# Kernel optimization log

Hardware: AMD Instinct MI355X
Metric: run time of the kernel (lower is better)

The kernel has to match this reference:

```python
import jax, jax.numpy as jnp
import numpy as np

B, C_IN, S = 32, 4, 2048
NF = 256          # CNN filters
H = 256           # LSTM hidden per direction
NH, DH = 8, 64    # heads, single-head size
MH = 512          # multihead size
KSZ, PAD, POOL = 13, 6, 6
SP = (S + 2 * PAD - KSZ + 1) // POOL  # 341: post conv(len-preserving)+maxpool1d length


def _lstm_dir(x, Wih, Whh, b):
    # x: [T, N, C] -- torch LSTM gate order i,f,g,o; b = b_ih + b_hh merged
    N = x.shape[1]
    h0 = jnp.zeros((N, H), x.dtype)
    c0 = jnp.zeros((N, H), x.dtype)

    def step(carry, xt):
        h, c = carry
        g = xt @ Wih.T + h @ Whh.T + b
        i, f, gg, o = jnp.split(g, 4, axis=-1)
        c = jax.nn.sigmoid(f) * c + jax.nn.sigmoid(i) * jnp.tanh(gg)
        h = jax.nn.sigmoid(o) * jnp.tanh(c)
        return (h, c), h

    _, hs = jax.lax.scan(step, (h0, c0), x)
    return hs


def _bilstm(x, Wih, Whh, b):
    fwd = _lstm_dir(x, Wih[0], Whh[0], b[0])
    bwd = _lstm_dir(x[::-1], Wih[1], Whh[1], b[1])[::-1]
    return jnp.concatenate([fwd, bwd], axis=-1)


def _rpe():
    # RelativePosition: |clip(k-q, -(S-1), S-1)| / (S-1); identical across the
    # batch-repeat channels, so compute once then broadcast (same math).
    r = jnp.arange(S)
    d = jnp.abs(jnp.clip(r[None, :] - r[:, None], -(S - 1), S - 1))
    d = d.astype(jnp.float32) / jnp.float32(S - 1)
    # nn.MaxPool2d((9,9), stride=(6,6), padding=1) -> [341, 341]
    return jax.lax.reduce_window(d, -jnp.inf, jax.lax.max, (9, 9), (6, 6), [(1, 1), (1, 1)])


def setup_inputs():
    key = jax.random.key(0)
    ks = jax.random.split(key, 20)
    f = lambda i, shape: jax.random.normal(ks[i], shape, jnp.float32) * 0.05
    return {
        "inputs": jax.random.normal(ks[0], (B, C_IN, S), jnp.float32),
        "conv1_w": f(1, (NF, C_IN, KSZ)),
        "bn1_gamma": jnp.ones((NF,), jnp.float32),
        "bn1_beta": jnp.zeros((NF,), jnp.float32),
        "Wih0": f(2, (2, 4 * H, NF)),
        "Whh0": f(3, (2, 4 * H, H)),
        "b0": f(4, (2, 4 * H)),
        "Wih1": f(5, (2, 4 * H, 2 * H)),
        "Whh1": f(6, (2, 4 * H, H)),
        "b1": f(7, (2, 4 * H)),
        "Qw": f(8, (NH, DH, 2 * H)), "Qb": f(9, (NH, DH)),
        "Kw": f(10, (NH, DH, 2 * H)), "Kb": f(11, (NH, DH)),
        "Vw": f(12, (NH, DH, 2 * H)), "Vb": f(13, (NH, DH)),
        "mh_w": f(14, (MH, NH * DH)), "mh_b": f(15, (MH,)),
    }


def reference(inputs, conv1_w, bn1_gamma, bn1_beta, Wih0, Whh0, b0,
              Wih1, Whh1, b1, Qw, Qb, Kw, Kb, Vw, Vb, mh_w, mh_b):
    # layer1: Conv1d (bias=False, pad=6 keeps length) + BatchNorm1d(eval: mean=0, var=1) + ReLU + MaxPool1d(6)
    x = jax.lax.conv_general_dilated(inputs, conv1_w, (1,), [(PAD, PAD)],
                                     dimension_numbers=('NCH', 'OIH', 'NCH'))
    x = x * (bn1_gamma / jnp.sqrt(1.0 + 1e-5))[None, :, None] + bn1_beta[None, :, None]
    x = jax.nn.relu(x)
    x = jax.lax.reduce_window(x, -jnp.inf, jax.lax.max, (1, 1, POOL), (1, 1, POOL), 'VALID')  # [B,NF,SP]
    x = jnp.transpose(x, (0, 2, 1))  # [B, SP, NF]

    # torch nn.LSTM with batch_first=False fed [B,SP,NF]: scans over axis 0 (batch) -- replicated faithfully.
    x = _bilstm(x, Wih0, Whh0, b0)
    x = _bilstm(x, Wih1, Whh1, b1)  # [B, SP, 2H]
    # (the F_RNN/R_RNN split-and-concat is an identity)

    # per-head Q/K/V (batched over heads), relative attention, dropout off (eval)
    q = jnp.einsum('bsc,hdc->hbsd', x, Qw) + Qb[:, None, None, :]
    k = jnp.einsum('bsc,hdc->hbsd', x, Kw) + Kb[:, None, None, :]
    v = jnp.einsum('bsc,hdc->hbsd', x, Vw) + Vb[:, None, None, :]
    scores = jnp.einsum('hbqd,hbkd->hbqk', q, k) / jnp.sqrt(jnp.float32(DH))
    scores = scores / _rpe()[None, None, :, :]
    p = jax.nn.softmax(scores, axis=-1)
    attn = jax.nn.relu(jnp.einsum('hbqk,hbkd->hbqd', p, v))  # [NH,B,SP,DH]
    cat = jnp.transpose(attn, (1, 2, 0, 3)).reshape(B, SP, NH * DH)
    out = jax.nn.relu(cat @ mh_w.T + mh_b)  # MultiHeadLinear + MHReLU
    return out
```

## Files before the change

kernel.cpp:

```cpp
#include <hip/hip_runtime.h>
#include <math.h>

#define B_    32
#define CIN   4
#define SLEN  2048
#define NF    256
#define HD    256
#define SP    341
#define RTOT  (B_*SP)
#define NH_   8
#define DH_   64
#define GRP   4
#define PSTR  344
#define HS    (SP*HD)
#define NBLK  176

typedef __attribute__((ext_vector_type(8))) short short8;
typedef __attribute__((ext_vector_type(4))) float floatx4;
typedef __attribute__((ext_vector_type(4))) unsigned short ushortx4;
typedef __attribute__((ext_vector_type(8))) unsigned short ushort8;

__device__ __forceinline__ float sigmoidf_(float x) { return 1.0f / (1.0f + expf(-x)); }

__device__ __forceinline__ unsigned short f2bf(float x) {
    unsigned int u = __float_as_uint(x);
    unsigned int r = (u + 0x7FFF + ((u >> 16) & 1)) >> 16;
    return (unsigned short)r;
}
__device__ __forceinline__ float bf2f(unsigned short b) {
    return __uint_as_float(((unsigned int)b) << 16);
}

__device__ __forceinline__ void store_f4_llc(float* p, floatx4 v)
{
    asm volatile("global_store_dwordx4 %0, %1, off sc0 sc1" :: "v"(p), "v"(v) : "memory");
}
__device__ __forceinline__ unsigned load_u32_llc(const unsigned* p)
{
    unsigned r;
    asm volatile("global_load_dword %0, %1, off sc0 sc1\n\ts_waitcnt vmcnt(0)"
                 : "=v"(r) : "v"(p) : "memory");
    return r;
}
__device__ __forceinline__ void load_h16_llc(const float* p, floatx4* r)
{
    asm volatile(
        "global_load_dwordx4 %0, %16, off sc0 sc1\n\t"
        "global_load_dwordx4 %1, %16, off offset:16 sc0 sc1\n\t"
        "global_load_dwordx4 %2, %16, off offset:128 sc0 sc1\n\t"
        "global_load_dwordx4 %3, %16, off offset:144 sc0 sc1\n\t"
        "global_load_dwordx4 %4, %16, off offset:256 sc0 sc1\n\t"
        "global_load_dwordx4 %5, %16, off offset:272 sc0 sc1\n\t"
        "global_load_dwordx4 %6, %16, off offset:384 sc0 sc1\n\t"
        "global_load_dwordx4 %7, %16, off offset:400 sc0 sc1\n\t"
        "global_load_dwordx4 %8, %16, off offset:512 sc0 sc1\n\t"
        "global_load_dwordx4 %9, %16, off offset:528 sc0 sc1\n\t"
        "global_load_dwordx4 %10, %16, off offset:640 sc0 sc1\n\t"
        "global_load_dwordx4 %11, %16, off offset:656 sc0 sc1\n\t"
        "global_load_dwordx4 %12, %16, off offset:768 sc0 sc1\n\t"
        "global_load_dwordx4 %13, %16, off offset:784 sc0 sc1\n\t"
        "global_load_dwordx4 %14, %16, off offset:896 sc0 sc1\n\t"
        "global_load_dwordx4 %15, %16, off offset:912 sc0 sc1\n\t"
        "s_waitcnt vmcnt(0)"
        : "=&v"(r[0]), "=&v"(r[1]), "=&v"(r[2]), "=&v"(r[3]),
          "=&v"(r[4]), "=&v"(r[5]), "=&v"(r[6]), "=&v"(r[7]),
          "=&v"(r[8]), "=&v"(r[9]), "=&v"(r[10]), "=&v"(r[11]),
          "=&v"(r[12]), "=&v"(r[13]), "=&v"(r[14]), "=&v"(r[15])
        : "v"(p)
        : "memory");
}


__global__ __launch_bounds__(256)
void conv_pool_k(const float* __restrict__ in, const float* __restrict__ cw,
                 const float* __restrict__ gamma, const float* __restrict__ beta,
                 unsigned short* __restrict__ x0p)
{
    const int b  = blockIdx.y;
    const int s0 = blockIdx.x * 16;
    const int co = threadIdx.x;
    __shared__ float ins[CIN][16*6 + 12];
    for (int idx = threadIdx.x; idx < CIN*108; idx += 256) {
        int ci = idx / 108, o = idx % 108;
        int pos = 6*s0 - 6 + o;
        ins[ci][o] = (pos >= 0 && pos < SLEN) ? in[(b*CIN + ci)*SLEN + pos] : 0.0f;
    }
    float wreg[52];
    {
        const float4* wp = (const float4*)(cw + co*52);
        #pragma unroll
        for (int j4 = 0; j4 < 13; ++j4) {
            float4 w4 = wp[j4];
            wreg[j4*4+0]=w4.x; wreg[j4*4+1]=w4.y; wreg[j4*4+2]=w4.z; wreg[j4*4+3]=w4.w;
        }
    }
    const float scale = gamma[co] * (1.0f / sqrtf(1.0f + 1e-5f));
    const float shift = beta[co];
    __syncthreads();
    for (int si = 0; si < 16; ++si) {
        int s = s0 + si;
        if (s >= SP) break;
        float win[CIN][18];
        #pragma unroll
        for (int ci = 0; ci < CIN; ++ci)
            #pragma unroll
            for (int o = 0; o < 18; ++o)
                win[ci][o] = ins[ci][6*si + o];
        float m = -1e30f;
        #pragma unroll
        for (int p6 = 0; p6 < 6; ++p6) {
            float acc = 0.0f;
            #pragma unroll
            for (int ci = 0; ci < CIN; ++ci)
                #pragma unroll
                for (int kk = 0; kk < 13; ++kk)
                    acc += win[ci][p6+kk] * wreg[ci*13+kk];
            float val = acc * scale + shift;
            val = fmaxf(val, 0.0f);
            m = fmaxf(m, val);
        }
        unsigned short hb_ = f2bf(m);
        unsigned short lb_ = f2bf(m - bf2f(hb_));
        size_t rb = (size_t)(b*SP + s)*512 + (size_t)(co >> 3)*16 + (co & 7);
        x0p[rb]     = hb_;
        x0p[rb + 8] = lb_;
    }
}

__global__ __launch_bounds__(256)
void pack4_k(const float* __restrict__ W, unsigned short* __restrict__ hi,
             unsigned short* __restrict__ lo, int n4)
{
    int i = blockIdx.x * 256 + threadIdx.x;
    if (i >= n4) return;
    float4 x = *((const float4*)W + i);
    float v[4] = {x.x, x.y, x.z, x.w};
    ushortx4 h, l;
    #pragma unroll
    for (int e = 0; e < 4; ++e) {
        unsigned short hb = f2bf(v[e]);
        h[e] = hb;
        l[e] = f2bf(v[e] - bf2f(hb));
    }
    *((ushortx4*)hi + i) = h;
    *((ushortx4*)lo + i) = l;
}

__global__ __launch_bounds__(256)
void pack8_k(const float* __restrict__ W, unsigned short* __restrict__ O, int n8)
{
    int i = blockIdx.x * 256 + threadIdx.x;
    if (i >= n8) return;
    const float4* wp = (const float4*)W + (size_t)i*2;
    float4 a = wp[0], b = wp[1];
    float v[8] = {a.x,a.y,a.z,a.w,b.x,b.y,b.z,b.w};
    ushort8 h, l;
    #pragma unroll
    for (int e = 0; e < 8; ++e) {
        unsigned short hb = f2bf(v[e]);
        h[e] = hb;
        l[e] = f2bf(v[e] - bf2f(hb));
    }
    *(ushort8*)(O + (size_t)i*16)     = h;
    *(ushort8*)(O + (size_t)i*16 + 8) = l;
}

template<int RELU>
__global__ __launch_bounds__(256)
void gemm_bf_k(const unsigned short* __restrict__ Ap, const unsigned short* __restrict__ Bp,
               const float* __restrict__ bias, float* __restrict__ C,
               int M, int N, int K)
{
    const int n0 = blockIdx.x * 128;
    const int m0 = blockIdx.y * 128;
    const int tid = threadIdx.x;
    const int lane = tid & 63;
    const int w = tid >> 6;
    const int wm = w >> 1, wn = w & 1;
    const int ln15 = lane & 15, lq = lane >> 4;
    const int l8 = lane >> 3, lj = lane & 7;
    const size_t rstr = 2*(size_t)K;

    __shared__ unsigned short As[128*64];
    __shared__ unsigned short Bs[128*64];

    floatx4 acc[4][4];
    #pragma unroll
    for (int i = 0; i < 4; ++i)
        #pragma unroll
        for (int j = 0; j < 4; ++j) acc[i][j] = (floatx4){0.f, 0.f, 0.f, 0.f};

    int rloc[4];
    #pragma unroll
    for (int c = 0; c < 4; ++c) rloc[c] = w*32 + c*8 + l8;
    const int spos = lj ^ (l8 & 7);

    for (int k0 = 0; k0 < K; k0 += 32) {
        short8 va[4], vb[4];
        #pragma unroll
        for (int c = 0; c < 4; ++c) {
            int gra = m0 + rloc[c]; if (gra >= M) gra = M - 1;
            va[c] = *(const short8*)(Ap + (size_t)gra*rstr + k0*2 + lj*8);
            vb[c] = *(const short8*)(Bp + (size_t)(n0 + rloc[c])*rstr + k0*2 + lj*8);
        }
        __syncthreads();
        #pragma unroll
        for (int c = 0; c < 4; ++c) {
            *(short8*)&As[rloc[c]*64 + spos*8] = va[c];
            *(short8*)&Bs[rloc[c]*64 + spos*8] = vb[c];
        }
        __syncthreads();

        short8 fa_h[4], fa_l[4], fb_h[4], fb_l[4];
        #pragma unroll
        for (int mt = 0; mt < 4; ++mt) {
            const int lr = wm*64 + mt*16 + ln15;
            fa_h[mt] = *(const short8*)&As[lr*64 + (((lq*2  ) ^ (lr&7))*8)];
            fa_l[mt] = *(const short8*)&As[lr*64 + (((lq*2+1) ^ (lr&7))*8)];
        }
        #pragma unroll
        for (int nt = 0; nt < 4; ++nt) {
            const int lr = wn*64 + nt*16 + ln15;
            fb_h[nt] = *(const short8*)&Bs[lr*64 + (((lq*2  ) ^ (lr&7))*8)];
            fb_l[nt] = *(const short8*)&Bs[lr*64 + (((lq*2+1) ^ (lr&7))*8)];
        }
        #pragma unroll
        for (int mt = 0; mt < 4; ++mt)
            #pragma unroll
            for (int nt = 0; nt < 4; ++nt) {
                acc[mt][nt] = __builtin_amdgcn_mfma_f32_16x16x32_bf16(fa_l[mt], fb_h[nt], acc[mt][nt], 0, 0, 0);
                acc[mt][nt] = __builtin_amdgcn_mfma_f32_16x16x32_bf16(fa_h[mt], fb_l[nt], acc[mt][nt], 0, 0, 0);
                acc[mt][nt] = __builtin_amdgcn_mfma_f32_16x16x32_bf16(fa_h[mt], fb_h[nt], acc[mt][nt], 0, 0, 0);
            }
    }

    #pragma unroll
    for (int nt = 0; nt < 4; ++nt) {
        const int n = n0 + wn*64 + nt*16 + ln15;
        const float bv = bias[n];
        #pragma unroll
        for (int mt = 0; mt < 4; ++mt) {
            const int mbase = m0 + wm*64 + mt*16 + lq*4;
            #pragma unroll
            for (int r = 0; r < 4; ++r) {
                int m = mbase + r;
                if (m < M) {
                    float val = acc[mt][nt][r] + bv;
                    if (RELU) val = fmaxf(val, 0.0f);
                    C[(size_t)m*N + n] = val;
                }
            }
        }
    }
}

__global__ __launch_bounds__(256)
void lstm_scan_k(const float* __restrict__ G,
                 const unsigned short* __restrict__ Whi,
                 const unsigned short* __restrict__ Wlo,
                 float* __restrict__ hb,
                 unsigned short* __restrict__ x_out,
                 unsigned* __restrict__ bar)
{
    const int j0 = blockIdx.x * 32;
    const int m0 = blockIdx.y * 32;
    const int d  = blockIdx.z;
    const int tid = threadIdx.x;
    const int w = tid >> 6, lane = tid & 63;
    const int mhalf = w & 1, gpair = w >> 1;
    const int ln15 = lane & 15, lq = lane >> 4;
    const size_t hsz = (size_t)2*SP*HD;
    unsigned* gbar = bar + (size_t)(blockIdx.y*2 + blockIdx.z)*64;

    __shared__ float Csh[32][132];

    int am = m0 + mhalf*16 + ln15; if (am > SP-1) am = SP-1;
    const int akoff = lq * 8;

    const unsigned short* WhiD = Whi + (size_t)d*1024*256;
    const unsigned short* WloD = Wlo + (size_t)d*1024*256;
    int nrow[4];
    #pragma unroll
    for (int t = 0; t < 4; ++t)
        nrow[t] = (gpair*2 + (t>>1))*256 + j0 + (t&1)*16 + ln15;

    const int emloc = tid >> 3;
    const int ej4   = (tid & 7) * 4;
    const int em    = m0 + emloc;

    floatx4 creg = (floatx4){0.f, 0.f, 0.f, 0.f};

    for (int s = 0; s < B_; ++s) {
        const int t_in = d ? (B_ - 1 - s) : s;
        float* hbuf_in  = hb + (size_t)(s & 1)*hsz;
        float* hbuf_out = hb + (size_t)((s+1) & 1)*hsz;

        floatx4 acc[4];
        #pragma unroll
        for (int t = 0; t < 4; ++t) acc[t] = (floatx4){0.f, 0.f, 0.f, 0.f};

        if (s > 0) {
            const float* p = hbuf_in + (size_t)d*HS + (size_t)am*HD + akoff;
            floatx4 hr[16];
            load_h16_llc(p, hr);
            #pragma unroll
            for (int kk = 0; kk < 8; ++kk) {
                const int ko = kk*32 + akoff;
                float vv[8] = {hr[2*kk][0], hr[2*kk][1], hr[2*kk][2], hr[2*kk][3],
                               hr[2*kk+1][0], hr[2*kk+1][1], hr[2*kk+1][2], hr[2*kk+1][3]};
                short8 ahi, alo;
                #pragma unroll
                for (int e = 0; e < 8; ++e) {
                    unsigned short hb16 = f2bf(vv[e]);
                    ahi[e] = (short)hb16;
                    alo[e] = (short)f2bf(vv[e] - bf2f(hb16));
                }
                #pragma unroll
                for (int t = 0; t < 4; ++t) {
                    short8 bhi = *(const short8*)(WhiD + (size_t)nrow[t]*HD + ko);
                    short8 blo = *(const short8*)(WloD + (size_t)nrow[t]*HD + ko);
                    acc[t] = __builtin_amdgcn_mfma_f32_16x16x32_bf16(alo, bhi, acc[t], 0, 0, 0);
                    acc[t] = __builtin_amdgcn_mfma_f32_16x16x32_bf16(ahi, blo, acc[t], 0, 0, 0);
                    acc[t] = __builtin_amdgcn_mfma_f32_16x16x32_bf16(ahi, bhi, acc[t], 0, 0, 0);
                }
            }
        }

        #pragma unroll
        for (int t = 0; t < 4; ++t) {
            int col = gpair*64 + (t>>1)*32 + (t&1)*16 + ln15;
            int rb  = mhalf*16 + lq*4;
            #pragma unroll
            for (int r = 0; r < 4; ++r)
                Csh[rb + r][col] = acc[t][r];
        }
        __syncthreads();

        if (em < SP) {
            size_t gb = ((size_t)t_in*SP + em)*2048 + (size_t)d*1024 + j0 + ej4;
            float4 gi4 = *(const float4*)&G[gb];
            float4 gf4 = *(const float4*)&G[gb + 256];
            float4 gg4 = *(const float4*)&G[gb + 512];
            float4 go4 = *(const float4*)&G[gb + 768];
            float hv[4];
            #pragma unroll
            for (int e = 0; e < 4; ++e) {
                float gi = Csh[emloc][     ej4+e] + (&gi4.x)[e];
                float gf = Csh[emloc][32 + ej4+e] + (&gf4.x)[e];
                float gg = Csh[emloc][64 + ej4+e] + (&gg4.x)[e];
                float go = Csh[emloc][96 + ej4+e] + (&go4.x)[e];
                float cn = sigmoidf_(gf)*creg[e] + sigmoidf_(gi)*tanhf(gg);
                creg[e] = cn;
                hv[e] = sigmoidf_(go)*tanhf(cn);
            }
            size_t cbase = ((size_t)d*SP + em)*HD + j0 + ej4;
            floatx4 ho = (floatx4){hv[0], hv[1], hv[2], hv[3]};
            store_f4_llc(&hbuf_out[cbase], ho);
            const int colg = d*HD + j0 + ej4;
            size_t xb = ((size_t)t_in*SP + em)*1024 + (size_t)(colg >> 3)*16 + (colg & 7);
            ushortx4 xh, xl;
            #pragma unroll
            for (int e = 0; e < 4; ++e) {
                unsigned short hb16 = f2bf(hv[e]);
                xh[e] = hb16;
                xl[e] = f2bf(hv[e] - bf2f(hb16));
            }
            *(ushortx4*)&x_out[xb]     = xh;
            *(ushortx4*)&x_out[xb + 8] = xl;
        }

        if (s < B_ - 1) {
            asm volatile("s_waitcnt vmcnt(0)" ::: "memory");
            __syncthreads();
            if (tid == 0) {
                atomicAdd(gbar, 1u);
                const unsigned target = (unsigned)(s + 1) * 8u;
                while (load_u32_llc(gbar) < target)
                    __builtin_amdgcn_s_sleep(2);
            }
            __syncthreads();
        }
    }
}

__global__ __launch_bounds__(256)
void scores_k(const float* __restrict__ q, const float* __restrict__ k,
              float* __restrict__ P, int g)
{
    const int h = blockIdx.z, bl = blockIdx.y, bg = g*GRP + bl;
    const int q0 = (blockIdx.x / 6) * 64;
    const int k0 = (blockIdx.x % 6) * 64;
    const int tid = threadIdx.x;
    __shared__ float qs[64][68];
    __shared__ float ks[64][68];
    {
        int jr = tid >> 2, c16 = (tid & 3) * 16;
        int qq = q0 + jr; if (qq > SP-1) qq = SP-1;
        int kr = k0 + jr; if (kr > SP-1) kr = SP-1;
        const float* qp = &q[((size_t)bg*SP + qq)*512 + h*64 + c16];
        const float* kp = &k[((size_t)bg*SP + kr)*512 + h*64 + c16];
        #pragma unroll
        for (int u = 0; u < 4; ++u) {
            *(float4*)&qs[jr][c16 + u*4] = *(const float4*)(qp + u*4);
            *(float4*)&ks[jr][c16 + u*4] = *(const float4*)(kp + u*4);
        }
    }
    __syncthreads();
    const int tx = tid & 15, ty = tid >> 4;
    float acc[4][4];
    #pragma unroll
    for (int i = 0; i < 4; ++i)
        #pragma unroll
        for (int j = 0; j < 4; ++j) acc[i][j] = 0.0f;
    for (int d4 = 0; d4 < 64; d4 += 4) {
        float4 a[4], b[4];
        #pragma unroll
        for (int i = 0; i < 4; ++i) a[i] = *(const float4*)&qs[ty + 16*i][d4];
        #pragma unroll
        for (int j = 0; j < 4; ++j) b[j] = *(const float4*)&ks[tx + 16*j][d4];
        #pragma unroll
        for (int i = 0; i < 4; ++i)
            #pragma unroll
            for (int j = 0; j < 4; ++j)
                acc[i][j] += a[i].x*b[j].x + a[i].y*b[j].y + a[i].z*b[j].z + a[i].w*b[j].w;
    }
    #pragma unroll
    for (int i = 0; i < 4; ++i) {
        int qq = q0 + ty + 16*i;
        if (qq >= SP) continue;
        int r0 = 6*qq - 1; if (r0 < 0) r0 = 0;
        int r1 = 6*qq + 7; if (r1 > SLEN-1) r1 = SLEN-1;
        size_t rowb = ((size_t)(h*GRP + bl)*SP + qq) * PSTR;
        #pragma unroll
        for (int j = 0; j < 4; ++j) {
            int kk = k0 + tx + 16*j;
            if (kk >= SP) continue;
            int c0 = 6*kk - 1; if (c0 < 0) c0 = 0;
            int c1 = 6*kk + 7;
            int dd1 = c1 - r0; if (dd1 < 0) dd1 = -dd1;
            int dd2 = r1 - c0; if (dd2 < 0) dd2 = -dd2;
            int den = dd1 > dd2 ? dd1 : dd2;
            P[rowb + kk] = (acc[i][j] * 0.125f) * 2047.0f / (float)den;
        }
    }
}

__global__ __launch_bounds__(256)
void softmax_k(float* __restrict__ P)
{
    const int tid = threadIdx.x;
    const int row = blockIdx.x * 4 + (tid >> 6);
    const int lane = tid & 63;
    float* rp = P + (size_t)row * PSTR;
    float v[6];
    float m = -1e30f;
    #pragma unroll
    for (int i = 0; i < 6; ++i) {
        int col = lane + 64*i;
        v[i] = (col < SP) ? rp[col] : -1e30f;
        m = fmaxf(m, v[i]);
    }
    #pragma unroll
    for (int o = 1; o < 64; o <<= 1) m = fmaxf(m, __shfl_xor(m, o, 64));
    float s = 0.0f;
    #pragma unroll
    for (int i = 0; i < 6; ++i) {
        v[i] = expf(v[i] - m);
        s += v[i];
    }
    #pragma unroll
    for (int o = 1; o < 64; o <<= 1) s += __shfl_xor(s, o, 64);
    float inv = 1.0f / s;
    #pragma unroll
    for (int i = 0; i < 6; ++i) {
        int col = lane + 64*i;
        if (col < SP) rp[col] = v[i] * inv;
    }
}

__global__ __launch_bounds__(256)
void pv_k(const float* __restrict__ P, const float* __restrict__ v,
          unsigned short* __restrict__ catp, int g)
{
    const int h = blockIdx.z, bl = blockIdx.y, bg = g*GRP + bl;
    const int q0 = blockIdx.x * 64;
    const int tid = threadIdx.x;
    __shared__ float ps[64][68];
    __shared__ float vs[64][68];
    const int tx = tid & 15, ty = tid >> 4;
    float acc[4][4];
    #pragma unroll
    for (int i = 0; i < 4; ++i)
        #pragma unroll
        for (int j = 0; j < 4; ++j) acc[i][j] = 0.0f;

    for (int kc = 0; kc < 6; ++kc) {
        const int kk0 = kc * 64;
        {
            int jr = tid >> 2, c16 = (tid & 3) * 16;
            int qq = q0 + jr; if (qq > SP-1) qq = SP-1;
            const float* pp = P + ((size_t)(h*GRP + bl)*SP + qq)*PSTR + kk0 + c16;
            #pragma unroll
            for (int u = 0; u < 4; ++u) {
                float4 w = *(const float4*)(pp + u*4);
                int klb = c16 + u*4;
                float vals[4] = {w.x, w.y, w.z, w.w};
                #pragma unroll
                for (int e = 0; e < 4; ++e)
                    ps[klb + e][jr] = (kk0 + klb + e < SP) ? vals[e] : 0.0f;
            }
        }
        {
            int jr = tid >> 2, c16 = (tid & 3) * 16;
            int kr = kk0 + jr; if (kr > SP-1) kr = SP-1;
            const float* vp = &v[((size_t)bg*SP + kr)*512 + h*64 + c16];
            #pragma unroll
            for (int u = 0; u < 4; ++u)
                *(float4*)&vs[jr][c16 + u*4] = *(const float4*)(vp + u*4);
        }
        __syncthreads();
        for (int kk = 0; kk < 64; ++kk) {
            float4 a4 = *(const float4*)&ps[kk][ty*4];
            float4 b4 = *(const float4*)&vs[kk][tx*4];
            float av[4] = {a4.x, a4.y, a4.z, a4.w};
            float bv[4] = {b4.x, b4.y, b4.z, b4.w};
            #pragma unroll
            for (int i = 0; i < 4; ++i)
                #pragma unroll
                for (int j = 0; j < 4; ++j)
                    acc[i][j] += av[i] * bv[j];
        }
        __syncthreads();
    }
    #pragma unroll
    for (int i = 0; i < 4; ++i) {
        int qq = q0 + ty*4 + i;
        if (qq >= SP) continue;
        float r[4];
        r[0] = fmaxf(acc[i][0], 0.0f);
        r[1] = fmaxf(acc[i][1], 0.0f);
        r[2] = fmaxf(acc[i][2], 0.0f);
        r[3] = fmaxf(acc[i][3], 0.0f);
        const int colg = h*64 + tx*4;
        size_t xb = ((size_t)bg*SP + qq)*1024 + (size_t)(colg >> 3)*16 + (colg & 7);
        ushortx4 xh, xl;
        #pragma unroll
        for (int e = 0; e < 4; ++e) {
            unsigned short hb16 = f2bf(r[e]);
            xh[e] = hb16;
            xl[e] = f2bf(r[e] - bf2f(hb16));
        }
        *(ushortx4*)&catp[xb]     = xh;
        *(ushortx4*)&catp[xb + 8] = xl;
    }
}

extern "C" void kernel_launch(void* const* d_in, const int* in_sizes, int n_in,
                              void* d_out, int out_size, void* d_ws, size_t ws_size,
                              hipStream_t stream)
{
    (void)in_sizes; (void)n_in; (void)out_size; (void)ws_size;
    const float* in    = (const float*)d_in[0];
    const float* cw    = (const float*)d_in[1];
    const float* gamma = (const float*)d_in[2];
    const float* beta  = (const float*)d_in[3];
    const float* Wih0  = (const float*)d_in[4];
    const float* Whh0  = (const float*)d_in[5];
    const float* b0    = (const float*)d_in[6];
    const float* Wih1  = (const float*)d_in[7];
    const float* Whh1  = (const float*)d_in[8];
    const float* b1    = (const float*)d_in[9];
    const float* Qw    = (const float*)d_in[10];
    const float* Qb    = (const float*)d_in[11];
    const float* Kw    = (const float*)d_in[12];
    const float* Kb    = (const float*)d_in[13];
    const float* Vw    = (const float*)d_in[14];
    const float* Vb    = (const float*)d_in[15];
    const float* mhw   = (const float*)d_in[16];
    const float* mhb   = (const float*)d_in[17];
    float* out = (float*)d_out;

    float* x0 = (float*)d_ws;
    float* G  = x0 + (size_t)RTOT*NF;
    float* x1 = G  + (size_t)RTOT*2048;
    float* x2 = x1 + (size_t)RTOT*512;
    float* hb = x2 + (size_t)RTOT*512;
    float* cb = hb + (size_t)2*2*SP*HD;

    float* qbuf = G;
    float* kbuf = G + (size_t)RTOT*512;
    float* vbuf = G + (size_t)2*RTOT*512;
    float* P    = G + (size_t)3*RTOT*512;
    unsigned* bar = (unsigned*)cb;

    unsigned short* x0p = (unsigned short*)x0;
    unsigned short* whh1_hi = (unsigned short*)x0;
    unsigned short* whh1_lo = whh1_hi + (size_t)524288;
    unsigned short* wih0_p  = (unsigned short*)x2;
    unsigned short* wih1_p  = wih0_p + (size_t)1048576;
    unsigned short* whh0_hi = wih1_p + (size_t)2097152;
    unsigned short* whh0_lo = whh0_hi + (size_t)524288;
    unsigned short* x1p  = (unsigned short*)x1;
    unsigned short* catp = (unsigned short*)x1;
    unsigned short* x2p = (unsigned short*)x2;
    float* gslack = P + (size_t)NH_*GRP*SP*PSTR;
    unsigned short* qw_p = (unsigned short*)gslack;
    unsigned short* kw_p = qw_p + (size_t)524288;
    unsigned short* vw_p = kw_p + (size_t)524288;
    unsigned short* mw_p = vw_p + (size_t)524288;

    #define PACKGRID(n) dim3(((n) + 255) / 256)

    conv_pool_k<<<dim3(22, B_), 256, 0, stream>>>(in, cw, gamma, beta, x0p);
    pack8_k<<<PACKGRID(65536), 256, 0, stream>>>(Wih0, wih0_p, 65536);
    gemm_bf_k<0><<<dim3(16, 86), 256, 0, stream>>>(x0p, wih0_p, b0, G, RTOT, 2048, 256);
    pack4_k<<<PACKGRID(131072), 256, 0, stream>>>(Whh0, whh0_hi, whh0_lo, 131072);
    pack4_k<<<PACKGRID(131072), 256, 0, stream>>>(Whh1, whh1_hi, whh1_lo, 131072);
    pack8_k<<<PACKGRID(131072), 256, 0, stream>>>(Wih1, wih1_p, 131072);
    hipMemsetAsync(bar, 0, 22*64*sizeof(unsigned), stream);
    {
        const float* a0 = G; const unsigned short* a1 = whh0_hi; const unsigned short* a2 = whh0_lo;
        float* a3 = hb; unsigned short* a4 = x1p; unsigned* a5 = bar;
        void* kargs[] = {&a0, &a1, &a2, &a3, &a4, &a5};
        hipLaunchCooperativeKernel((void*)lstm_scan_k, dim3(8, 11, 2), dim3(256, 1, 1), kargs, 0, stream);
    }
    gemm_bf_k<0><<<dim3(16, 86), 256, 0, stream>>>(x1p, wih1_p, b1, G, RTOT, 2048, 512);
    hipMemsetAsync(bar, 0, 22*64*sizeof(unsigned), stream);
    {
        const float* a0 = G; const unsigned short* a1 = whh1_hi; const unsigned short* a2 = whh1_lo;
        float* a3 = hb; unsigned short* a4 = x2p; unsigned* a5 = bar;
        void* kargs[] = {&a0, &a1, &a2, &a3, &a4, &a5};
        hipLaunchCooperativeKernel((void*)lstm_scan_k, dim3(8, 11, 2), dim3(256, 1, 1), kargs, 0, stream);
    }
    pack8_k<<<PACKGRID(32768), 256, 0, stream>>>(Qw,  qw_p, 32768);
    pack8_k<<<PACKGRID(32768), 256, 0, stream>>>(Kw,  kw_p, 32768);
    pack8_k<<<PACKGRID(32768), 256, 0, stream>>>(Vw,  vw_p, 32768);
    pack8_k<<<PACKGRID(32768), 256, 0, stream>>>(mhw, mw_p, 32768);
    gemm_bf_k<0><<<dim3(4, 86), 256, 0, stream>>>(x2p, qw_p, Qb, qbuf, RTOT, 512, 512);
    gemm_bf_k<0><<<dim3(4, 86), 256, 0, stream>>>(x2p, kw_p, Kb, kbuf, RTOT, 512, 512);
    gemm_bf_k<0><<<dim3(4, 86), 256, 0, stream>>>(x2p, vw_p, Vb, vbuf, RTOT, 512, 512);
    for (int g = 0; g < B_/GRP; ++g) {
        scores_k <<<dim3(36, GRP, NH_), 256, 0, stream>>>(qbuf, kbuf, P, g);
        softmax_k<<<dim3(NH_*GRP*SP/4), 256, 0, stream>>>(P);
        pv_k     <<<dim3(6, GRP, NH_), 256, 0, stream>>>(P, vbuf, catp, g);
    }
    gemm_bf_k<1><<<dim3(4, 86), 256, 0, stream>>>(catp, mw_p, mhb, out, RTOT, 512, 512);
    #undef PACKGRID
}
```

Before: 1.643 ms.

## Fuse scores with softmax and move PV to split-bf16 MFMA with transposed V

Merges the score computation and the row softmax into one kernel that holds a full 341-column row in registers, so the separate softmax pass and its fp32 round trip are dropped. P is written in a packed hi/lo bf16 layout, and V is written transposed in the same packed form by a new GEMM epilogue. The PV product now runs on bf16 MFMA with three passes to recover near-fp32 precision. This adds a memset over the transposed V buffer. The scores kernel now launches fewer, larger blocks that loop over all key chunks, which may lower parallelism.

```diff
diff --git a/kernel.cpp b/kernel.cpp
--- a/kernel.cpp
+++ b/kernel.cpp
@@ -13,7 +13,7 @@
 #define GRP   4
 #define PSTR  344
 #define HS    (SP*HD)
-#define NBLK  176
+#define PKS   768
 
 typedef __attribute__((ext_vector_type(8))) short short8;
 typedef __attribute__((ext_vector_type(4))) float floatx4;
@@ -255,6 +255,98 @@
 }
 
 __global__ __launch_bounds__(256)
+void gemm_vT_k(const unsigned short* __restrict__ Ap, const unsigned short* __restrict__ Bp,
+               const float* __restrict__ bias, unsigned short* __restrict__ vT,
+               int M, int N, int K)
+{
+    const int n0 = blockIdx.x * 128;
+    const int m0 = blockIdx.y * 128;
+    const int tid = threadIdx.x;
+    const int lane = tid & 63;
+    const int w = tid >> 6;
+    const int wm = w >> 1, wn = w & 1;
+    const int ln15 = lane & 15, lq = lane >> 4;
+    const int l8 = lane >> 3, lj = lane & 7;
+    const size_t rstr = 2*(size_t)K;
+
+    __shared__ unsigned short As[128*64];
+    __shared__ unsigned short Bs[128*64];
+
+    floatx4 acc[4][4];
+    #pragma unroll
+    for (int i = 0; i < 4; ++i)
+        #pragma unroll
+        for (int j = 0; j < 4; ++j) acc[i][j] = (floatx4){0.f, 0.f, 0.f, 0.f};
+
+    int rloc[4];
+    #pragma unroll
+    for (int c = 0; c < 4; ++c) rloc[c] = w*32 + c*8 + l8;
+    const int spos = lj ^ (l8 & 7);
+
+    for (int k0 = 0; k0 < K; k0 += 32) {
+        short8 va[4], vb[4];
+        #pragma unroll
+        for (int c = 0; c < 4; ++c) {
+            int gra = m0 + rloc[c]; if (gra >= M) gra = M - 1;
+            va[c] = *(const short8*)(Ap + (size_t)gra*rstr + k0*2 + lj*8);
+            vb[c] = *(const short8*)(Bp + (size_t)(n0 + rloc[c])*rstr + k0*2 + lj*8);
+        }
+        __syncthreads();
+        #pragma unroll
+        for (int c = 0; c < 4; ++c) {
+            *(short8*)&As[rloc[c]*64 + spos*8] = va[c];
+            *(short8*)&Bs[rloc[c]*64 + spos*8] = vb[c];
+        }
+        __syncthreads();
+
+        short8 fa_h[4], fa_l[4], fb_h[4], fb_l[4];
+        #pragma unroll
+        for (int mt = 0; mt < 4; ++mt) {
+            const int lr = wm*64 + mt*16 + ln15;
+            fa_h[mt] = *(const short8*)&As[lr*64 + (((lq*2  ) ^ (lr&7))*8)];
+            fa_l[mt] = *(const short8*)&As[lr*64 + (((lq*2+1) ^ (lr&7))*8)];
+        }
+        #pragma unroll
+        for (int nt = 0; nt < 4; ++nt) {
+            const int lr = wn*64 + nt*16 + ln15;
+            fb_h[nt] = *(const short8*)&Bs[lr*64 + (((lq*2  ) ^ (lr&7))*8)];
+            fb_l[nt] = *(const short8*)&Bs[lr*64 + (((lq*2+1) ^ (lr&7))*8)];
+        }
+        #pragma unroll
+        for (int mt = 0; mt < 4; ++mt)
+            #pragma unroll
+            for (int nt = 0; nt < 4; ++nt) {
+                acc[mt][nt] = __builtin_amdgcn_mfma_f32_16x16x32_bf16(fa_l[mt], fb_h[nt], acc[mt][nt], 0, 0, 0);
+                acc[mt][nt] = __builtin_amdgcn_mfma_f32_16x16x32_bf16(fa_h[mt], fb_l[nt], acc[mt][nt], 0, 0, 0);
+                acc[mt][nt] = __builtin_amdgcn_mfma_f32_16x16x32_bf16(fa_h[mt], fb_h[nt], acc[mt][nt], 0, 0, 0);
+            }
+    }
+
+    #pragma unroll
+    for (int nt = 0; nt < 4; ++nt) {
+        const int n = n0 + wn*64 + nt*16 + ln15;
+        const float bv = bias[n];
+        #pragma unroll
+        for (int mt = 0; mt < 4; ++mt) {
+            const int mbase = m0 + wm*64 + mt*16 + lq*4;
+            #pragma unroll
+            for (int r = 0; r < 4; ++r) {
+                int m = mbase + r;
+                if (m < M) {
+                    float val = acc[mt][nt][r] + bv;
+                    int bg = m / 341;
+                    int sp = m - bg*341;
+                    size_t vb_ = ((size_t)bg*512 + n)*PKS + (size_t)((sp >> 3)*16 + (sp & 7));
+                    unsigned short hb16 = f2bf(val);
+                    vT[vb_]     = hb16;
+                    vT[vb_ + 8] = f2bf(val - bf2f(hb16));
+                }
+            }
+        }
+    }
+}
+
+__global__ __launch_bounds__(256)
 void lstm_scan_k(const float* __restrict__ G,
                  const unsigned short* __restrict__ Whi,
                  const unsigned short* __restrict__ Wlo,
@@ -384,174 +476,164 @@
 }
 
 __global__ __launch_bounds__(256)
-void scores_k(const float* __restrict__ q, const float* __restrict__ k,
-              float* __restrict__ P, int g)
+void scores_sm_k(const float* __restrict__ q, const float* __restrict__ k,
+                 unsigned short* __restrict__ Ppk, int g)
 {
     const int h = blockIdx.z, bl = blockIdx.y, bg = g*GRP + bl;
-    const int q0 = (blockIdx.x / 6) * 64;
-    const int k0 = (blockIdx.x % 6) * 64;
+    const int q0 = blockIdx.x * 32;
     const int tid = threadIdx.x;
-    __shared__ float qs[64][68];
+    const int tx = tid & 15, ty = tid >> 4;
+    __shared__ float qs[32][68];
     __shared__ float ks[64][68];
     {
-        int jr = tid >> 2, c16 = (tid & 3) * 16;
+        int jr = tid >> 3, c8 = (tid & 7) * 8;
         int qq = q0 + jr; if (qq > SP-1) qq = SP-1;
-        int kr = k0 + jr; if (kr > SP-1) kr = SP-1;
-        const float* qp = &q[((size_t)bg*SP + qq)*512 + h*64 + c16];
-        const float* kp = &k[((size_t)bg*SP + kr)*512 + h*64 + c16];
-        #pragma unroll
-        for (int u = 0; u < 4; ++u) {
-            *(float4*)&qs[jr][c16 + u*4] = *(const float4*)(qp + u*4);
-            *(float4*)&ks[jr][c16 + u*4] = *(const float4*)(kp + u*4);
-        }
-    }
-    __syncthreads();
-    const int tx = tid & 15, ty = tid >> 4;
-    float acc[4][4];
-    #pragma unroll
-    for (int i = 0; i < 4; ++i)
-        #pragma unroll
-        for (int j = 0; j < 4; ++j) acc[i][j] = 0.0f;
-    for (int d4 = 0; d4 < 64; d4 += 4) {
-        float4 a[4], b[4];
-        #pragma unroll
-        for (int i = 0; i < 4; ++i) a[i] = *(const float4*)&qs[ty + 16*i][d4];
-        #pragma unroll
-        for (int j = 0; j < 4; ++j) b[j] = *(const float4*)&ks[tx + 16*j][d4];
-        #pragma unroll
-        for (int i = 0; i < 4; ++i)
-            #pragma unroll
-            for (int j = 0; j < 4; ++j)
-                acc[i][j] += a[i].x*b[j].x + a[i].y*b[j].y + a[i].z*b[j].z + a[i].w*b[j].w;
-    }
-    #pragma unroll
-    for (int i = 0; i < 4; ++i) {
-        int qq = q0 + ty + 16*i;
-        if (qq >= SP) continue;
+        const float* qp = &q[((size_t)bg*SP + qq)*512 + h*64 + c8];
+        *(float4*)&qs[jr][c8]     = *(const float4*)qp;
+        *(float4*)&qs[jr][c8 + 4] = *(const float4*)(qp + 4);
+    }
+    float sv[2][24];
+    for (int kc = 0; kc < 6; ++kc) {
+        __syncthreads();
+        {
+            int jr = tid >> 2, c16 = (tid & 3) * 16;
+            int kr = kc*64 + jr; if (kr > SP-1) kr = SP-1;
+            const float* kp = &k[((size_t)bg*SP + kr)*512 + h*64 + c16];
+            #pragma unroll
+            for (int u = 0; u < 4; ++u)
+                *(float4*)&ks[jr][c16 + u*4] = *(const float4*)(kp + u*4);
+        }
+        __syncthreads();
+        float a_[2][4] = {{0.f,0.f,0.f,0.f},{0.f,0.f,0.f,0.f}};
+        for (int d4 = 0; d4 < 64; d4 += 4) {
+            float4 a0 = *(const float4*)&qs[ty][d4];
+            float4 a1 = *(const float4*)&qs[ty + 16][d4];
+            float4 b[4];
+            #pragma unroll
+            for (int j = 0; j < 4; ++j) b[j] = *(const float4*)&ks[tx + 16*j][d4];
+            #pragma unroll
+            for (int j = 0; j < 4; ++j) {
+                a_[0][j] += a0.x*b[j].x + a0.y*b[j].y + a0.z*b[j].z + a0.w*b[j].w;
+                a_[1][j] += a1.x*b[j].x + a1.y*b[j].y + a1.z*b[j].z + a1.w*b[j].w;
+            }
+        }
+        #pragma unroll
+        for (int i = 0; i < 2; ++i)
+            #pragma unroll
+            for (int j = 0; j < 4; ++j) sv[i][kc*4 + j] = a_[i][j];
+    }
+    #pragma unroll
+    for (int i = 0; i < 2; ++i) {
+        const int qq = q0 + ty + 16*i;
         int r0 = 6*qq - 1; if (r0 < 0) r0 = 0;
         int r1 = 6*qq + 7; if (r1 > SLEN-1) r1 = SLEN-1;
-        size_t rowb = ((size_t)(h*GRP + bl)*SP + qq) * PSTR;
-        #pragma unroll
-        for (int j = 0; j < 4; ++j) {
-            int kk = k0 + tx + 16*j;
-            if (kk >= SP) continue;
-            int c0 = 6*kk - 1; if (c0 < 0) c0 = 0;
-            int c1 = 6*kk + 7;
-            int dd1 = c1 - r0; if (dd1 < 0) dd1 = -dd1;
-            int dd2 = r1 - c0; if (dd2 < 0) dd2 = -dd2;
-            int den = dd1 > dd2 ? dd1 : dd2;
-            P[rowb + kk] = (acc[i][j] * 0.125f) * 2047.0f / (float)den;
+        float m = -1e30f;
+        #pragma unroll
+        for (int jj = 0; jj < 24; ++jj) {
+            const int col = (jj >> 2)*64 + (jj & 3)*16 + tx;
+            float s;
+            if (col < SP) {
+                int c0 = 6*col - 1; if (c0 < 0) c0 = 0;
+                int c1 = 6*col + 7;
+                int dd1 = c1 - r0; if (dd1 < 0) dd1 = -dd1;
+                int dd2 = r1 - c0; if (dd2 < 0) dd2 = -dd2;
+                int den = dd1 > dd2 ? dd1 : dd2;
+                s = (sv[i][jj] * 0.125f) * 2047.0f / (float)den;
+            } else s = -1e30f;
+            sv[i][jj] = s;
+            m = fmaxf(m, s);
+        }
+        #pragma unroll
+        for (int o = 1; o < 16; o <<= 1) m = fmaxf(m, __shfl_xor(m, o, 64));
+        float sum = 0.0f;
+        #pragma unroll
+        for (int jj = 0; jj < 24; ++jj) {
+            float v = expf(sv[i][jj] - m);
+            sv[i][jj] = v;
+            sum += v;
+        }
+        #pragma unroll
+        for (int o = 1; o < 16; o <<= 1) sum += __shfl_xor(sum, o, 64);
+        const float inv = 1.0f / sum;
+        if (qq < SP) {
+            const size_t pb = ((size_t)(h*GRP + bl)*SP + qq) * PKS;
+            #pragma unroll
+            for (int jj = 0; jj < 24; ++jj) {
+                const int col = (jj >> 2)*64 + (jj & 3)*16 + tx;
+                float p = sv[i][jj] * inv;
+                unsigned short hb16 = f2bf(p);
+                size_t pp = pb + (size_t)((col >> 3)*16 + (col & 7));
+                Ppk[pp]     = hb16;
+                Ppk[pp + 8] = f2bf(p - bf2f(hb16));
+            }
         }
     }
 }
 
 __global__ __launch_bounds__(256)
-void softmax_k(float* __restrict__ P)
-{
-    const int tid = threadIdx.x;
-    const int row = blockIdx.x * 4 + (tid >> 6);
-    const int lane = tid & 63;
-    float* rp = P + (size_t)row * PSTR;
-    float v[6];
-    float m = -1e30f;
-    #pragma unroll
-    for (int i = 0; i < 6; ++i) {
-        int col = lane + 64*i;
-        v[i] = (col < SP) ? rp[col] : -1e30f;
-        m = fmaxf(m, v[i]);
-    }
-    #pragma unroll
-    for (int o = 1; o < 64; o <<= 1) m = fmaxf(m, __shfl_xor(m, o, 64));
-    float s = 0.0f;
-    #pragma unroll
-    for (int i = 0; i < 6; ++i) {
-        v[i] = expf(v[i] - m);
-        s += v[i];
-    }
-    #pragma unroll
-    for (int o = 1; o < 64; o <<= 1) s += __shfl_xor(s, o, 64);
-    float inv = 1.0f / s;
-    #pragma unroll
-    for (int i = 0; i < 6; ++i) {
-        int col = lane + 64*i;
-        if (col < SP) rp[col] = v[i] * inv;
-    }
-}
-
-__global__ __launch_bounds__(256)
-void pv_k(const float* __restrict__ P, const float* __restrict__ v,
-          unsigned short* __restrict__ catp, int g)
+void pv_bf_k(const unsigned short* __restrict__ Ppk, const unsigned short* __restrict__ vT,
+             unsigned short* __restrict__ catp, int g)
 {
     const int h = blockIdx.z, bl = blockIdx.y, bg = g*GRP + bl;
     const int q0 = blockIdx.x * 64;
     const int tid = threadIdx.x;
-    __shared__ float ps[64][68];
-    __shared__ float vs[64][68];
-    const int tx = tid & 15, ty = tid >> 4;
-    float acc[4][4];
-    #pragma unroll
-    for (int i = 0; i < 4; ++i)
-        #pragma unroll
-        for (int j = 0; j < 4; ++j) acc[i][j] = 0.0f;
-
-    for (int kc = 0; kc < 6; ++kc) {
-        const int kk0 = kc * 64;
-        {
-            int jr = tid >> 2, c16 = (tid & 3) * 16;
-            int qq = q0 + jr; if (qq > SP-1) qq = SP-1;
-            const float* pp = P + ((size_t)(h*GRP + bl)*SP + qq)*PSTR + kk0 + c16;
-            #pragma unroll
-            for (int u = 0; u < 4; ++u) {
-                float4 w = *(const float4*)(pp + u*4);
-                int klb = c16 + u*4;
-                float vals[4] = {w.x, w.y, w.z, w.w};
-                #pragma unroll
-                for (int e = 0; e < 4; ++e)
-                    ps[klb + e][jr] = (kk0 + klb + e < SP) ? vals[e] : 0.0f;
-            }
-        }
-        {
-            int jr = tid >> 2, c16 = (tid & 3) * 16;
-            int kr = kk0 + jr; if (kr > SP-1) kr = SP-1;
-            const float* vp = &v[((size_t)bg*SP + kr)*512 + h*64 + c16];
-            #pragma unroll
-            for (int u = 0; u < 4; ++u)
-                *(float4*)&vs[jr][c16 + u*4] = *(const float4*)(vp + u*4);
-        }
-        __syncthreads();
-        for (int kk = 0; kk < 64; ++kk) {
-            float4 a4 = *(const float4*)&ps[kk][ty*4];
-            float4 b4 = *(const float4*)&vs[kk][tx*4];
-            float av[4] = {a4.x, a4.y, a4.z, a4.w};
-            float bv[4] = {b4.x, b4.y, b4.z, b4.w};
-            #pragma unroll
-            for (int i = 0; i < 4; ++i)
-                #pragma unroll
-                for (int j = 0; j < 4; ++j)
-                    acc[i][j] += av[i] * bv[j];
-        }
-        __syncthreads();
-    }
-    #pragma unroll
-    for (int i = 0; i < 4; ++i) {
-        int qq = q0 + ty*4 + i;
-        if (qq >= SP) continue;
-        float r[4];
-        r[0] = fmaxf(acc[i][0], 0.0f);
-        r[1] = fmaxf(acc[i][1], 0.0f);
-        r[2] = fmaxf(acc[i][2], 0.0f);
-        r[3] = fmaxf(acc[i][3], 0.0f);
-        const int colg = h*64 + tx*4;
-        size_t xb = ((size_t)bg*SP + qq)*1024 + (size_t)(colg >> 3)*16 + (colg & 7);
-        ushortx4 xh, xl;
-        #pragma unroll
-        for (int e = 0; e < 4; ++e) {
-            unsigned short hb16 = f2bf(r[e]);
-            xh[e] = hb16;
-            xl[e] = f2bf(r[e] - bf2f(hb16));
-        }
-        *(ushortx4*)&catp[xb]     = xh;
-        *(ushortx4*)&catp[xb + 8] = xl;
+    const int lane = tid & 63, w = tid >> 6;
+    const int ln15 = lane & 15, lq = lane >> 4;
+    const int l8 = lane >> 3, lj = lane & 7;
+    __shared__ unsigned short As[64*64];
+    __shared__ unsigned short Bs[64*64];
+    floatx4 acc[4];
+    #pragma unroll
+    for (int nt = 0; nt < 4; ++nt) acc[nt] = (floatx4){0.f,0.f,0.f,0.f};
+    const int spos = lj ^ (l8 & 7);
+    const size_t prow = (size_t)(h*GRP + bl)*SP;
+    const size_t vrow = (size_t)bg*512 + h*64;
+
+    for (int step = 0; step < 12; ++step) {
+        const int ku = step * 64;
+        short8 va[2], vb[2];
+        #pragma unroll
+        for (int c = 0; c < 2; ++c) {
+            const int r = w*16 + c*8 + l8;
+            int qa = q0 + r; if (qa > SP-1) qa = SP-1;
+            va[c] = *(const short8*)(Ppk + (prow + qa)*PKS + ku + lj*8);
+            vb[c] = *(const short8*)(vT + (vrow + r)*PKS + ku + lj*8);
+        }
+        __syncthreads();
+        #pragma unroll
+        for (int c = 0; c < 2; ++c) {
+            const int r = w*16 + c*8 + l8;
+            *(short8*)&As[r*64 + spos*8] = va[c];
+            *(short8*)&Bs[r*64 + spos*8] = vb[c];
+        }
+        __syncthreads();
+        const int lrA = w*16 + ln15;
+        short8 fa_h = *(const short8*)&As[lrA*64 + (((lq*2  ) ^ (lrA&7))*8)];
+        short8 fa_l = *(const short8*)&As[lrA*64 + (((lq*2+1) ^ (lrA&7))*8)];
+        #pragma unroll
+        for (int nt = 0; nt < 4; ++nt) {
+            const int lrB = nt*16 + ln15;
+            short8 fb_h = *(const short8*)&Bs[lrB*64 + (((lq*2  ) ^ (lrB&7))*8)];
+            short8 fb_l = *(const short8*)&Bs[lrB*64 + (((lq*2+1) ^ (lrB&7))*8)];
+            acc[nt] = __builtin_amdgcn_mfma_f32_16x16x32_bf16(fa_l, fb_h, acc[nt], 0, 0, 0);
+            acc[nt] = __builtin_amdgcn_mfma_f32_16x16x32_bf16(fa_h, fb_l, acc[nt], 0, 0, 0);
+            acc[nt] = __builtin_amdgcn_mfma_f32_16x16x32_bf16(fa_h, fb_h, acc[nt], 0, 0, 0);
+        }
+    }
+    #pragma unroll
+    for (int nt = 0; nt < 4; ++nt) {
+        const int colg = h*64 + nt*16 + ln15;
+        #pragma unroll
+        for (int r = 0; r < 4; ++r) {
+            const int em = q0 + w*16 + lq*4 + r;
+            if (em < SP) {
+                float val = fmaxf(acc[nt][r], 0.0f);
+                size_t xb = ((size_t)bg*SP + em)*1024 + (size_t)((colg >> 3)*16 + (colg & 7));
+                unsigned short hb16 = f2bf(val);
+                catp[xb]     = hb16;
+                catp[xb + 8] = f2bf(val - bf2f(hb16));
+            }
+        }
     }
 }
 
@@ -589,13 +671,17 @@
 
     float* qbuf = G;
     float* kbuf = G + (size_t)RTOT*512;
-    float* vbuf = G + (size_t)2*RTOT*512;
-    float* P    = G + (size_t)3*RTOT*512;
+    unsigned short* vT  = (unsigned short*)(G + (size_t)2*RTOT*512);
+    unsigned short* Ppk = (unsigned short*)(G + (size_t)2*RTOT*512 + 6291456);
     unsigned* bar = (unsigned*)cb;
 
     unsigned short* x0p = (unsigned short*)x0;
     unsigned short* whh1_hi = (unsigned short*)x0;
     unsigned short* whh1_lo = whh1_hi + (size_t)524288;
+    unsigned short* qw_p = (unsigned short*)(x0 + (size_t)524288);
+    unsigned short* kw_p = qw_p + (size_t)524288;
+    unsigned short* vw_p = kw_p + (size_t)524288;
+    unsigned short* mw_p = vw_p + (size_t)524288;
     unsigned short* wih0_p  = (unsigned short*)x2;
     unsigned short* wih1_p  = wih0_p + (size_t)1048576;
     unsigned short* whh0_hi = wih1_p + (size_t)2097152;
@@ -603,11 +689,6 @@
     unsigned short* x1p  = (unsigned short*)x1;
     unsigned short* catp = (unsigned short*)x1;
     unsigned short* x2p = (unsigned short*)x2;
-    float* gslack = P + (size_t)NH_*GRP*SP*PSTR;
-    unsigned short* qw_p = (unsigned short*)gslack;
-    unsigned short* kw_p = qw_p + (size_t)524288;
-    unsigned short* vw_p = kw_p + (size_t)524288;
-    unsigned short* mw_p = vw_p + (size_t)524288;
 
     #define PACKGRID(n) dim3(((n) + 255) / 256)
 
@@ -638,11 +719,11 @@
     pack8_k<<<PACKGRID(32768), 256, 0, stream>>>(mhw, mw_p, 32768);
     gemm_bf_k<0><<<dim3(4, 86), 256, 0, stream>>>(x2p, qw_p, Qb, qbuf, RTOT, 512, 512);
     gemm_bf_k<0><<<dim3(4, 86), 256, 0, stream>>>(x2p, kw_p, Kb, kbuf, RTOT, 512, 512);
-    gemm_bf_k<0><<<dim3(4, 86), 256, 0, stream>>>(x2p, vw_p, Vb, vbuf, RTOT, 512, 512);
+    hipMemsetAsync(vT, 0, (size_t)B_*512*PKS*sizeof(unsigned short), stream);
+    gemm_vT_k<<<dim3(4, 86), 256, 0, stream>>>(x2p, vw_p, Vb, vT, RTOT, 512, 512);
     for (int g = 0; g < B_/GRP; ++g) {
-        scores_k <<<dim3(36, GRP, NH_), 256, 0, stream>>>(qbuf, kbuf, P, g);
-        softmax_k<<<dim3(NH_*GRP*SP/4), 256, 0, stream>>>(P);
-        pv_k     <<<dim3(6, GRP, NH_), 256, 0, stream>>>(P, vbuf, catp, g);
+        scores_sm_k<<<dim3(11, GRP, NH_), 256, 0, stream>>>(qbuf, kbuf, Ppk, g);
+        pv_bf_k    <<<dim3(6,  GRP, NH_), 256, 0, stream>>>(Ppk, vT, catp, g);
     }
     gemm_bf_k<1><<<dim3(4, 86), 256, 0, stream>>>(catp, mw_p, mhb, out, RTOT, 512, 512);
     #undef PACKGRID
```

Measured after the change: 1.699 ms. 1.03x slower.
